# Kernel tuning notes

Measured on AMD Instinct MI355X. Metric: run time of the kernel, lower is better.

## Reference

```python
import jax, jax.numpy as jnp
import numpy as np

EMBED = 1024
HEADS = 16
HEAD_DIM = EMBED // HEADS
LN_EPS = 1e-5
XNORM_GAMMA = 0.01


def xnorm(x, gamma):
    # x * gamma / ||x||_4 along last dim (keepdim)
    norm4 = jnp.sum(x ** 4, axis=-1, keepdims=True) ** 0.25
    return x * gamma / norm4


def setup_inputs() -> dict:
    key = jax.random.key(0)
    ks = jax.random.split(key, 12)
    B, S = 2, 2048
    sc_hd = 1.0 / np.sqrt(HEAD_DIM)
    sc_e = 1.0 / np.sqrt(EMBED)
    return {
        "value": jax.random.normal(ks[0], (B, S, EMBED), jnp.float32),
        "key": jax.random.normal(ks[1], (B, S, EMBED), jnp.float32),
        "query": jax.random.normal(ks[2], (B, S, EMBED), jnp.float32),
        # per-head projections, torch Linear convention: y = x @ W.T
        "Wq": jax.random.normal(ks[3], (HEAD_DIM, HEAD_DIM), jnp.float32) * sc_hd,
        "Wk": jax.random.normal(ks[4], (HEAD_DIM, HEAD_DIM), jnp.float32) * sc_hd,
        "Wv": jax.random.normal(ks[5], (HEAD_DIM, HEAD_DIM), jnp.float32) * sc_hd,
        "Wo": jax.random.normal(ks[6], (EMBED, EMBED), jnp.float32) * sc_e,
        "bo": jnp.zeros((EMBED,), jnp.float32),
        "ln_w": jnp.ones((EMBED,), jnp.float32),
        "ln_b": jnp.zeros((EMBED,), jnp.float32),
        "Wsq": jax.random.normal(ks[7], (EMBED, EMBED), jnp.float32) * sc_e,
        "bsq": jnp.zeros((EMBED,), jnp.float32),
    }


def reference(value, key, query, Wq, Wk, Wv, Wo, bo, ln_w, ln_b, Wsq, bsq):
    B, S, E = query.shape
    # split heads: [B, S, H, D]
    v = value.reshape(B, S, HEADS, HEAD_DIM)
    k = key.reshape(B, S, HEADS, HEAD_DIM)
    q = query.reshape(B, S, HEADS, HEAD_DIM)
    v = jnp.einsum('nshd,ed->nshe', v, Wv)
    k = jnp.einsum('nshd,ed->nshe', k, Wk)
    q = jnp.einsum('nshd,ed->nshe', q, Wq)
    # energy: [B, H, Sq, Sk]
    energy = jnp.einsum('nqhd,nkhd->nhqk', q, k)
    energy_n = xnorm(energy, XNORM_GAMMA)
    v_n = xnorm(v, XNORM_GAMMA)
    out = jnp.einsum('nhql,nlhd->nqhd', energy_n, v_n).reshape(B, S, E)
    attn = out @ Wo.T + bo
    # LayerNorm(attention + query) over embed dim
    x = attn + query
    mu = jnp.mean(x, axis=-1, keepdims=True)
    var = jnp.mean((x - mu) ** 2, axis=-1, keepdims=True)
    x = (x - mu) / jnp.sqrt(var + LN_EPS) * ln_w + ln_b
    # SE gating: x * sigmoid(Linear(x))
    gate = jax.nn.sigmoid(x @ Wsq.T + bsq)
    return x * gate
```

## Files before the change

kernel.cpp:

```cpp
#include <hip/hip_runtime.h>
#include <stdint.h>

#define B_ 2
#define S_ 2048
#define E_ 1024
#define H_ 16
#define HD_ 64
#define N_ (B_*S_)
#define BH_ (B_*H_)
#define GAMMA 0.01f

typedef __attribute__((ext_vector_type(8))) short bf16x8;
typedef __attribute__((ext_vector_type(4))) float f32x4;
typedef __attribute__((ext_vector_type(2))) float f32x2;
typedef __attribute__((ext_vector_type(16))) float f32x16;
typedef __attribute__((ext_vector_type(4))) unsigned int u32x4;
typedef unsigned short u16;
typedef unsigned int u32;

#define SWZ(row, kb) ((kb) ^ (((row)&7)<<4))

__device__ __forceinline__ u16 f2bf(float f){
  union { float f; u32 u; } v; v.f = f;
  return (u16)((v.u + 0x7FFFu + ((v.u>>16)&1u)) >> 16);
}

__device__ __forceinline__ float bf2f(u16 u){
  union { u32 u; float f; } v; v.u = ((u32)u)<<16; return v.f;
}

__device__ __forceinline__ u32 cvt_pk_bf16(float lo, float hi){
  u32 r; asm("v_cvt_pk_bf16_f32 %0, %1, %2" : "=v"(r) : "v"(lo), "v"(hi)); return r;
}

__device__ __forceinline__ uint4 pack8(float4 a, float4 b){
  uint4 r;
  r.x = (u32)f2bf(a.x) | ((u32)f2bf(a.y)<<16);
  r.y = (u32)f2bf(a.z) | ((u32)f2bf(a.w)<<16);
  r.z = (u32)f2bf(b.x) | ((u32)f2bf(b.y)<<16);
  r.w = (u32)f2bf(b.z) | ((u32)f2bf(b.w)<<16);
  return r;
}

__device__ __forceinline__ bf16x8 ldfrag(const unsigned char* base, int row, int kbyte){
  return *reinterpret_cast<const bf16x8*>(base + row*128 + SWZ(row, kbyte));
}
__device__ __forceinline__ bf16x8 ldfragV(const unsigned char* base, int row, int col){
  return *reinterpret_cast<const bf16x8*>(base + row*256 + (col ^ ((row&15)<<4)));
}

__device__ __forceinline__ void gl_lds16(const void* g, void* l){
  __builtin_amdgcn_global_load_lds(
      (const __attribute__((address_space(1))) unsigned int*)g,
      (__attribute__((address_space(3))) unsigned int*)l, 16, 0, 0);
}

__device__ __forceinline__ void proj_mfma(const unsigned char* X, const unsigned char* W,
                                          int wid, int l15, int g4, f32x4 acc[4])
{
  f32x4 z = {0.f,0.f,0.f,0.f};
  acc[0]=z; acc[1]=z; acc[2]=z; acc[3]=z;
  #pragma unroll
  for (int kk=0;kk<2;++kk){
    int kbyte = kk*64 + g4*16;
    bf16x8 a = ldfrag(X, wid*16 + l15, kbyte);
    #pragma unroll
    for (int t=0;t<4;++t){
      bf16x8 w = ldfrag(W, t*16 + l15, kbyte);
      acc[t] = __builtin_amdgcn_mfma_f32_16x16x32_bf16(a, w, acc[t], 0, 0, 0);
    }
  }
}

__global__ __launch_bounds__(256) void k_proj(
    const float* __restrict__ qin, const float* __restrict__ kin, const float* __restrict__ vin,
    const float* __restrict__ Wq, const float* __restrict__ Wk, const float* __restrict__ Wv,
    u16* __restrict__ qp, u16* __restrict__ kp, u16* __restrict__ vnT,
    const float* __restrict__ Wo, const float* __restrict__ Wsq,
    u16* __restrict__ wo16, u16* __restrict__ wsq16)
{
  __shared__ alignas(16) unsigned char sm[57344];
  if (blockIdx.y >= H_){
    int cblk = (blockIdx.y - H_)*64 + blockIdx.x;
    int n4 = (E_*E_)/4;
    for (int i = cblk*256 + threadIdx.x; i < 2*n4; i += 128*256){
      const float4* src; ushort4* dst; int j;
      if (i < n4){ src=(const float4*)Wo;  dst=(ushort4*)wo16;  j=i; }
      else       { src=(const float4*)Wsq; dst=(ushort4*)wsq16; j=i-n4; }
      float4 v = src[j];
      ushort4 p; p.x=f2bf(v.x); p.y=f2bf(v.y); p.z=f2bf(v.z); p.w=f2bf(v.w);
      dst[j] = p;
    }
    return;
  }
  const int XQ=0, XK=8192, XV=16384, WQS=24576, WKS=32768, WVS=40960, VT=49152;
  int tid = threadIdx.x, lane = tid&63, wid = tid>>6;
  int l15 = lane&15, g4 = lane>>4;
  int tb = blockIdx.x*64;
  int h  = blockIdx.y;
  int b  = tb >> 11;
  int sbase = tb & 2047;
  int bh = b*H_ + h;

  {
    int rl = tid>>2;
    int d0 = (tid&3)*16;
    const float* xs[3] = { qin, kin, vin };
    const float* wsrc[3] = { Wq, Wk, Wv };
    const int xoff[3] = {XQ,XK,XV}, woff[3] = {WQS,WKS,WVS};
    #pragma unroll
    for (int m3=0;m3<3;++m3){
      const float4* gx = reinterpret_cast<const float4*>(xs[m3] + (size_t)(tb+rl)*E_ + h*HD_ + d0);
      float4 a=gx[0], bb=gx[1], c=gx[2], d=gx[3];
      *(uint4*)(sm + xoff[m3] + rl*128 + SWZ(rl, d0*2))    = pack8(a,bb);
      *(uint4*)(sm + xoff[m3] + rl*128 + SWZ(rl, d0*2+16)) = pack8(c,d);
      const float4* gw = reinterpret_cast<const float4*>(wsrc[m3] + rl*64 + d0);
      float4 e=gw[0], f=gw[1], g2=gw[2], h2=gw[3];
      *(uint4*)(sm + woff[m3] + rl*128 + SWZ(rl, d0*2))    = pack8(e,f);
      *(uint4*)(sm + woff[m3] + rl*128 + SWZ(rl, d0*2+16)) = pack8(g2,h2);
    }
  }
  __syncthreads();

  f32x4 acc[4];
  proj_mfma(sm+XQ, sm+WQS, wid, l15, g4, acc);
  #pragma unroll
  for (int t=0;t<4;++t)
    #pragma unroll
    for (int r=0;r<4;++r){
      int tokl = wid*16 + g4*4 + r;
      qp[((size_t)bh*S_ + sbase + tokl)*HD_ + t*16 + l15] = f2bf(acc[t][r]);
    }
  proj_mfma(sm+XK, sm+WKS, wid, l15, g4, acc);
  #pragma unroll
  for (int t=0;t<4;++t)
    #pragma unroll
    for (int r=0;r<4;++r){
      int tokl = wid*16 + g4*4 + r;
      kp[((size_t)bh*S_ + sbase + tokl)*HD_ + t*16 + l15] = f2bf(acc[t][r]);
    }
  proj_mfma(sm+XV, sm+WVS, wid, l15, g4, acc);
  {
    float p4r[4] = {0.f,0.f,0.f,0.f};
    #pragma unroll
    for (int t=0;t<4;++t)
      #pragma unroll
      for (int r=0;r<4;++r){ float e = acc[t][r]; float e2 = e*e; p4r[r] += e2*e2; }
    #pragma unroll
    for (int r=0;r<4;++r){
      float p = p4r[r];
      p += __shfl_xor(p,1); p += __shfl_xor(p,2); p += __shfl_xor(p,4); p += __shfl_xor(p,8);
      p4r[r] = GAMMA / sqrtf(sqrtf(p));
    }
    #pragma unroll
    for (int t=0;t<4;++t)
      #pragma unroll
      for (int r=0;r<4;++r){
        int tokl = wid*16 + g4*4 + r;
        int dd = t*16 + l15;
        *(u16*)(sm + VT + dd*128 + SWZ(dd, tokl*2)) = f2bf(acc[t][r] * p4r[r]);
      }
  }
  __syncthreads();
  {
    int dd = tid>>2; int c2 = tid&3;
    size_t gbase = ((size_t)bh*HD_ + dd)*S_ + sbase + c2*16;
    uint4 v0 = *(const uint4*)(sm + VT + dd*128 + SWZ(dd, c2*32));
    uint4 v1 = *(const uint4*)(sm + VT + dd*128 + SWZ(dd, c2*32+16));
    *(uint4*)(vnT + gbase)     = v0;
    *(uint4*)(vnT + gbase + 8) = v1;
  }
}

__global__ __launch_bounds__(256, 2) void k_attn(
    const u16* __restrict__ qp, const u16* __restrict__ kp,
    const u16* __restrict__ vnT, u16* __restrict__ ao)
{
  __shared__ alignas(128) unsigned char sm[65536];
  char* smc = (char*)sm;
  int tid = threadIdx.x, lane = tid&63, wv = tid>>6;
  int l31 = lane&31, hi = lane>>5;
  int qi = wv>>1, kj = wv&1;
  int L = blockIdx.x;
  int xcd = L&7, iw = L>>3;
  int bh = xcd*4 + (iw>>4);
  int qx = iw&15;
  int qb = qx*128;
  int b = bh>>4, h = bh&15;
  const u16* Kb = kp  + (size_t)bh*S_*HD_;
  const u16* Vb = vnT + (size_t)bh*HD_*S_;
  const u16* Qb = qp  + (size_t)bh*S_*HD_;
  int q0 = qb + qi*64;

  bf16x8 qf[2][4];
  #pragma unroll
  for (int f=0;f<2;++f)
    #pragma unroll
    for (int kk=0;kk<4;++kk)
      qf[f][kk] = *reinterpret_cast<const bf16x8*>(Qb + (size_t)(q0 + f*32 + l31)*HD_ + kk*16 + hi*8);

  f32x16 z16 = {};
  f32x16 o[2][2];
  #pragma unroll
  for (int f=0;f<2;++f){ o[f][0] = z16; o[f][1] = z16; }
  f32x2 p4a[2] = {{0.f,0.f},{0.f,0.f}};
  f32x2 p4b[2] = {{0.f,0.f},{0.f,0.f}};

  const char* kSrcC[4]; const char* vSrcC[4];
  #pragma unroll
  for (int c=0;c<4;++c){
    int rk = wv*32 + c*8 + (lane>>3);
    int ck = ((lane&7)*16) ^ ((rk&7)<<4);
    kSrcC[c] = (const char*)Kb + (size_t)rk*128 + ck;
    int rv = wv*16 + c*4 + (lane>>4);
    int cv = ((lane&15)*16) ^ ((rv&15)<<4);
    vSrcC[c] = (const char*)Vb + (size_t)rv*4096 + cv;
  }

  auto STAGE = [&](int bsel, int kt){
    char* db = smc + bsel*32768 + wv*4096;
    #pragma unroll
    for (int c=0;c<4;++c) gl_lds16(kSrcC[c] + (size_t)kt*16384, db + c*1024);
    #pragma unroll
    for (int c=0;c<4;++c) gl_lds16(vSrcC[c] + (size_t)kt*256,   db + 16384 + c*1024);
  };

  auto PACK = [&](const f32x16& e, u32 (&w)[4][2], f32x2& pa){
    #pragma unroll
    for (int j=0;j<8;++j){
      const int g=j>>1, i=j&1;
      float a = e[4*g+2*i], c = e[4*g+2*i+1];
      f32x2 pr = {a, c};
      f32x2 e2;
      asm("v_pk_mul_f32 %0, %1, %1" : "=v"(e2) : "v"(pr));
      asm("v_pk_fma_f32 %0, %1, %1, %0" : "+v"(pa) : "v"(e2));
      w[g][i] = cvt_pk_bf16(a, c);
    }
  };
  auto AFRAG = [&](u32 (&w)[4][2], int s) -> bf16x8 {
    u32 a0 = w[2*s][0], b0 = w[2*s+1][0];
    u32 a1 = w[2*s][1], b1 = w[2*s+1][1];
    asm("v_permlane32_swap_b32 %0, %1" : "+v"(a0), "+v"(b0));
    asm("v_permlane32_swap_b32 %0, %1" : "+v"(a1), "+v"(b1));
    u32x4 fw = {a0, a1, b0, b1};
    return __builtin_bit_cast(bf16x8, fw);
  };

  auto QK = [&](const unsigned char* K_, int s2, f32x16& E0, f32x16& E1){
    bf16x8 ka[4];
    #pragma unroll
    for (int kk=0;kk<4;++kk) ka[kk] = ldfrag(K_, kj*64 + s2*32 + l31, kk*32 + hi*16);
    E0 = z16; E1 = z16;
    __builtin_amdgcn_s_setprio(1);
    #pragma unroll
    for (int kk=0;kk<4;++kk){
      E0 = __builtin_amdgcn_mfma_f32_32x32x16_bf16(ka[kk], qf[0][kk], E0, 0,0,0);
      E1 = __builtin_amdgcn_mfma_f32_32x32x16_bf16(ka[kk], qf[1][kk], E1, 0,0,0);
    }
    __builtin_amdgcn_s_setprio(0);
  };

  auto PVF = [&](const unsigned char* V_, int s2, u32 (&w0)[4][2], u32 (&w1)[4][2]){
    bf16x8 vb[2][2];
    #pragma unroll
    for (int s=0;s<2;++s){
      vb[s][0] = ldfragV(V_, l31,    kj*128 + s2*64 + s*32 + hi*16);
      vb[s][1] = ldfragV(V_, 32+l31, kj*128 + s2*64 + s*32 + hi*16);
    }
    __builtin_amdgcn_s_setprio(1);
    #pragma unroll
    for (int s=0;s<2;++s){
      bf16x8 ef0 = AFRAG(w0, s);
      bf16x8 ef1 = AFRAG(w1, s);
      o[0][0] = __builtin_amdgcn_mfma_f32_32x32x16_bf16(ef0, vb[s][0], o[0][0], 0,0,0);
      o[0][1] = __builtin_amdgcn_mfma_f32_32x32x16_bf16(ef0, vb[s][1], o[0][1], 0,0,0);
      o[1][0] = __builtin_amdgcn_mfma_f32_32x32x16_bf16(ef1, vb[s][0], o[1][0], 0,0,0);
      o[1][1] = __builtin_amdgcn_mfma_f32_32x32x16_bf16(ef1, vb[s][1], o[1][1], 0,0,0);
    }
    __builtin_amdgcn_s_setprio(0);
  };

  const int NT = S_/128;
  STAGE(0, 0); STAGE(1, 1);

  f32x16 eA0, eA1, eB0, eB1;
  u32 wA0[4][2], wA1[4][2], wB0[4][2], wB1[4][2];

  #pragma unroll 1
  for (int t=0; t<NT; ++t){
    if (t < NT-1) { asm volatile("s_waitcnt vmcnt(8)" ::: "memory"); }
    else          { asm volatile("s_waitcnt vmcnt(0)" ::: "memory"); }
    __builtin_amdgcn_s_barrier();
    asm volatile("" ::: "memory");
    const unsigned char* K_ = sm + (t&1)*32768;
    const unsigned char* V_ = K_ + 16384;

    QK(K_, 0, eA0, eA1);
    QK(K_, 1, eB0, eB1);
    PACK(eA0, wA0, p4a[0]);
    PACK(eA1, wA1, p4a[1]);
    PVF(V_, 0, wA0, wA1);
    PACK(eB0, wB0, p4b[0]);
    PACK(eB1, wB1, p4b[1]);
    PVF(V_, 1, wB0, wB1);

    asm volatile("" ::: "memory");
    __builtin_amdgcn_s_barrier();
    asm volatile("" ::: "memory");
    if (t+2 < NT) STAGE(t&1, t+2);
  }

  float p4f[2];
  #pragma unroll
  for (int f=0;f<2;++f) p4f[f] = p4a[f].x + p4a[f].y + p4b[f].x + p4b[f].y;

  __syncthreads();
  float* red  = (float*)smc;
  float* redp = (float*)(smc + 32768);
  if (kj==1){
    #pragma unroll
    for (int f=0;f<2;++f){
      #pragma unroll
      for (int ds=0;ds<2;++ds){
        float* dst = red + ((((qi*2+f)*2+ds)*64 + lane)*16);
        #pragma unroll
        for (int r4=0;r4<4;++r4)
          *(float4*)(dst + r4*4) = make_float4(o[f][ds][r4*4],o[f][ds][r4*4+1],o[f][ds][r4*4+2],o[f][ds][r4*4+3]);
      }
      redp[(qi*2+f)*64 + lane] = p4f[f];
    }
  }
  __syncthreads();
  if (kj==0){
    #pragma unroll
    for (int f=0;f<2;++f){
      #pragma unroll
      for (int ds=0;ds<2;++ds){
        const float* srcp = red + ((((qi*2+f)*2+ds)*64 + lane)*16);
        #pragma unroll
        for (int r4=0;r4<4;++r4){
          float4 t = *(const float4*)(srcp + r4*4);
          o[f][ds][r4*4]+=t.x; o[f][ds][r4*4+1]+=t.y; o[f][ds][r4*4+2]+=t.z; o[f][ds][r4*4+3]+=t.w;
        }
      }
      p4f[f] += redp[(qi*2+f)*64 + lane];
      p4f[f] += __shfl_xor(p4f[f], 32);
    }
    float sc0 = GAMMA * rsqrtf(sqrtf(p4f[0]));
    float sc1 = GAMMA * rsqrtf(sqrtf(p4f[1]));
    #pragma unroll
    for (int f=0;f<2;++f){
      #pragma unroll
      for (int r=0;r<16;++r){
        int qrow = (r&3) + 8*(r>>2) + 4*hi;
        float scr = __shfl(f==0 ? sc0 : sc1, qrow);
        size_t n = (size_t)b*S_ + q0 + f*32 + qrow;
        u16* dst = ao + n*E_ + h*HD_;
        dst[l31]    = f2bf(o[f][0][r] * scr);
        dst[32+l31] = f2bf(o[f][1][r] * scr);
      }
    }
  }
}

template<int MODE>
__global__ __launch_bounds__(256, 2) void k_gemm(
    const u16* __restrict__ A, const u16* __restrict__ Bw,
    const float* __restrict__ bias, const float* __restrict__ auxf,
    const u16* __restrict__ aux16, float* __restrict__ out32, u16* __restrict__ out16)
{
  __shared__ alignas(128) unsigned char sm[73728];
  char* smc = (char*)sm;
  int tid = threadIdx.x, lane = tid&63, wv = tid>>6;
  int l31 = lane&31, hi = lane>>5;
  int wr = wv>>1, wc = wv&1;
  int LL = (blockIdx.x & 7)*64 + (blockIdx.x >> 3);
  int mt = LL >> 4, nt = LL & 15;
  int m0 = mt*128, n0 = nt*64;

  int ric  = lane>>3;
  int colb = ((lane&7)*16) ^ ((ric&7)<<4);
  const char* aSrc[4]; const char* bSrc[2];
  #pragma unroll
  for (int j=0;j<4;++j)
    aSrc[j] = (const char*)A  + ((size_t)(m0 + wv*32 + 8*j + ric)*E_)*2 + colb;
  #pragma unroll
  for (int j=0;j<2;++j)
    bSrc[j] = (const char*)Bw + ((size_t)(n0 + wv*16 + 8*j + ric)*E_)*2 + colb;

  auto STAGE = [&](int bsel, int t){
    char* db = smc + bsel*24576;
    size_t kb2 = (size_t)t*128;
    #pragma unroll
    for (int j=0;j<4;++j) gl_lds16(aSrc[j] + kb2, db + (wv*4+j)*1024);
    #pragma unroll
    for (int j=0;j<2;++j) gl_lds16(bSrc[j] + kb2, db + 16384 + (wv*2+j)*1024);
  };

  f32x16 acc[2] = {{}, {}};

  const int NK = E_/64;
  STAGE(0, 0); STAGE(1, 1);

  #pragma unroll 1
  for (int t=0; t<NK; ++t){
    if (t < NK-1) { asm volatile("s_waitcnt vmcnt(6)" ::: "memory"); }
    else          { asm volatile("s_waitcnt vmcnt(0)" ::: "memory"); }
    __builtin_amdgcn_s_barrier();
    asm volatile("" ::: "memory");
    if (t+2 < NK) STAGE((t+2)%3, t+2);

    const unsigned char* Ap_ = sm + (t%3)*24576;
    const unsigned char* Bp_ = Ap_ + 16384;
    #pragma unroll
    for (int kk=0;kk<4;++kk){
      bf16x8 bfr = ldfrag(Bp_, wc*32 + l31, kk*32 + hi*16);
      bf16x8 af0 = ldfrag(Ap_, wr*64 + l31,      kk*32 + hi*16);
      bf16x8 af1 = ldfrag(Ap_, wr*64 + 32 + l31, kk*32 + hi*16);
      __builtin_amdgcn_s_setprio(1);
      acc[0] = __builtin_amdgcn_mfma_f32_32x32x16_bf16(af0, bfr, acc[0], 0,0,0);
      acc[1] = __builtin_amdgcn_mfma_f32_32x32x16_bf16(af1, bfr, acc[1], 0,0,0);
      __builtin_amdgcn_s_setprio(0);
    }
  }

  int col = n0 + wc*32 + l31;
  float bi = bias[col];
  #pragma unroll
  for (int rg=0;rg<2;++rg)
    #pragma unroll
    for (int r=0;r<16;++r){
      int mrow = m0 + wr*64 + rg*32 + (r&3) + 8*(r>>2) + 4*hi;
      size_t idx = (size_t)mrow*E_ + col;
      float v = acc[rg][r] + bi;
      if (MODE == 0){
        out16[idx] = f2bf(v + auxf[idx]);
      } else {
        float gg = 1.f/(1.f + __expf(-v));
        out32[idx] = bf2f(aux16[idx]) * gg;
      }
    }
}

__global__ __launch_bounds__(256) void k_ln(
    const u16* __restrict__ xin, const float* __restrict__ lnw, const float* __restrict__ lnb,
    u16* __restrict__ xout)
{
  __shared__ float red[8];
  __shared__ float stats[2];
  int row = blockIdx.x, tid = threadIdx.x;
  ushort4 xr = reinterpret_cast<const ushort4*>(xin + (size_t)row*E_)[tid];
  float x0 = bf2f(xr.x), x1 = bf2f(xr.y), x2 = bf2f(xr.z), x3 = bf2f(xr.w);
  float s  = x0 + x1 + x2 + x3;
  float s2 = x0*x0 + x1*x1 + x2*x2 + x3*x3;
  #pragma unroll
  for (int m=1;m<64;m<<=1){ s += __shfl_xor(s,m); s2 += __shfl_xor(s2,m); }
  if ((tid&63)==0){ red[tid>>6] = s; red[4+(tid>>6)] = s2; }
  __syncthreads();
  if (tid==0){
    float ts  = red[0]+red[1]+red[2]+red[3];
    float ts2 = red[4]+red[5]+red[6]+red[7];
    float mu  = ts * (1.f/E_);
    float var = ts2 * (1.f/E_) - mu*mu;
    stats[0] = mu; stats[1] = rsqrtf(var + 1e-5f);
  }
  __syncthreads();
  float mu = stats[0], rstd = stats[1];
  float4 w  = reinterpret_cast<const float4*>(lnw)[tid];
  float4 bb = reinterpret_cast<const float4*>(lnb)[tid];
  ushort4 p;
  p.x = f2bf((x0-mu)*rstd*w.x + bb.x);
  p.y = f2bf((x1-mu)*rstd*w.y + bb.y);
  p.z = f2bf((x2-mu)*rstd*w.z + bb.z);
  p.w = f2bf((x3-mu)*rstd*w.w + bb.w);
  reinterpret_cast<ushort4*>(xout + (size_t)row*E_)[tid] = p;
}

extern "C" void kernel_launch(void* const* d_in, const int* in_sizes, int n_in,
                              void* d_out, int out_size, void* d_ws, size_t ws_size,
                              hipStream_t stream)
{
  const float* value = (const float*)d_in[0];
  const float* key   = (const float*)d_in[1];
  const float* query = (const float*)d_in[2];
  const float* Wq    = (const float*)d_in[3];
  const float* Wk    = (const float*)d_in[4];
  const float* Wv    = (const float*)d_in[5];
  const float* Wo    = (const float*)d_in[6];
  const float* bo    = (const float*)d_in[7];
  const float* lnw   = (const float*)d_in[8];
  const float* lnb   = (const float*)d_in[9];
  const float* Wsq   = (const float*)d_in[10];
  const float* bsq   = (const float*)d_in[11];
  float* out = (float*)d_out;

  char* ws = (char*)d_ws;
  const size_t MB = 1ull<<20;
  u16*   qp     = (u16*)(ws + 0*MB);
  u16*   kp     = (u16*)(ws + 8*MB);
  u16*   vnT    = (u16*)(ws + 16*MB);
  u16*   ao     = (u16*)(ws + 24*MB);
  u16*   xres16 = (u16*)(ws + 8*MB);
  u16*   x16    = (u16*)(ws + 16*MB);
  u16*   wo16   = (u16*)(ws + 48*MB);
  u16*   wsq16  = (u16*)(ws + 50*MB);

  k_proj<<<dim3(N_/64, H_+2), 256, 0, stream>>>(query, key, value, Wq, Wk, Wv,
                                                qp, kp, vnT, Wo, Wsq, wo16, wsq16);
  k_attn<<<512, 256, 0, stream>>>(qp, kp, vnT, ao);
  k_gemm<0><<<512, 256, 0, stream>>>(ao, wo16, bo, query, (const u16*)nullptr, (float*)nullptr, xres16);
  k_ln  <<<N_, 256, 0, stream>>>(xres16, lnw, lnb, x16);
  k_gemm<1><<<512, 256, 0, stream>>>(x16, wsq16, bsq, (const float*)nullptr, x16, out, (u16*)nullptr);
}
```

Measured before the change: 108.6 us.

## Split attention key tiles across four waves per query pair with tree reduction

Doubles the attention block to 512 threads (8 waves), so each of the four key-split waves per query half handles 32 keys per tile instead of 64. Staging of K/V into LDS is spread over more waves, and the split-K partial outputs and norm sums are combined with a two-level LDS reduction. The aim is more waves per CU to hide MFMA and LDS latency, at the cost of extra reduction passes, more barriers, and possible register pressure under launch_bounds(512,4).

```diff
diff --git a/kernel.cpp b/kernel.cpp
--- a/kernel.cpp
+++ b/kernel.cpp
@@ -172,15 +172,16 @@
   }
 }
 
-__global__ __launch_bounds__(256, 2) void k_attn(
+__global__ __launch_bounds__(512, 4) void k_attn(
     const u16* __restrict__ qp, const u16* __restrict__ kp,
     const u16* __restrict__ vnT, u16* __restrict__ ao)
 {
   __shared__ alignas(128) unsigned char sm[65536];
+  __shared__ float p4s[2][256];
   char* smc = (char*)sm;
   int tid = threadIdx.x, lane = tid&63, wv = tid>>6;
   int l31 = lane&31, hi = lane>>5;
-  int qi = wv>>1, kj = wv&1;
+  int qi = wv>>2, kj = wv&3;
   int L = blockIdx.x;
   int xcd = L&7, iw = L>>3;
   int bh = xcd*4 + (iw>>4);
@@ -204,25 +205,23 @@
   #pragma unroll
   for (int f=0;f<2;++f){ o[f][0] = z16; o[f][1] = z16; }
   f32x2 p4a[2] = {{0.f,0.f},{0.f,0.f}};
-  f32x2 p4b[2] = {{0.f,0.f},{0.f,0.f}};
-
-  const char* kSrcC[4]; const char* vSrcC[4];
-  #pragma unroll
-  for (int c=0;c<4;++c){
-    int rk = wv*32 + c*8 + (lane>>3);
-    int ck = ((lane&7)*16) ^ ((rk&7)<<4);
-    kSrcC[c] = (const char*)Kb + (size_t)rk*128 + ck;
-    int rv = wv*16 + c*4 + (lane>>4);
-    int cv = ((lane&15)*16) ^ ((rv&15)<<4);
-    vSrcC[c] = (const char*)Vb + (size_t)rv*4096 + cv;
+
+  const char* kSrcC[2]; const char* vSrcC[2];
+  #pragma unroll
+  for (int c=0;c<2;++c){
+    int off = wv*2048 + c*1024 + lane*16;
+    int rk = off>>7, ck = off&127;
+    kSrcC[c] = (const char*)Kb + (size_t)rk*128 + (ck ^ ((rk&7)<<4));
+    int rv = off>>8, cv = off&255;
+    vSrcC[c] = (const char*)Vb + (size_t)rv*4096 + (cv ^ ((rv&15)<<4));
   }
 
   auto STAGE = [&](int bsel, int kt){
-    char* db = smc + bsel*32768 + wv*4096;
-    #pragma unroll
-    for (int c=0;c<4;++c) gl_lds16(kSrcC[c] + (size_t)kt*16384, db + c*1024);
-    #pragma unroll
-    for (int c=0;c<4;++c) gl_lds16(vSrcC[c] + (size_t)kt*256,   db + 16384 + c*1024);
+    char* db = smc + bsel*32768 + wv*2048;
+    #pragma unroll
+    for (int c=0;c<2;++c) gl_lds16(kSrcC[c] + (size_t)kt*16384, db + c*1024);
+    #pragma unroll
+    for (int c=0;c<2;++c) gl_lds16(vSrcC[c] + (size_t)kt*256,   db + 16384 + c*1024);
   };
 
   auto PACK = [&](const f32x16& e, u32 (&w)[4][2], f32x2& pa){
@@ -246,26 +245,40 @@
     return __builtin_bit_cast(bf16x8, fw);
   };
 
-  auto QK = [&](const unsigned char* K_, int s2, f32x16& E0, f32x16& E1){
+  const int NT = S_/128;
+  STAGE(0, 0); STAGE(1, 1);
+
+  u32 w0[4][2], w1[4][2];
+
+  #pragma unroll 1
+  for (int t=0; t<NT; ++t){
+    if (t < NT-1) { asm volatile("s_waitcnt vmcnt(4)" ::: "memory"); }
+    else          { asm volatile("s_waitcnt vmcnt(0)" ::: "memory"); }
+    __builtin_amdgcn_s_barrier();
+    asm volatile("" ::: "memory");
+    const unsigned char* K_ = sm + (t&1)*32768;
+    const unsigned char* V_ = K_ + 16384;
+
     bf16x8 ka[4];
     #pragma unroll
-    for (int kk=0;kk<4;++kk) ka[kk] = ldfrag(K_, kj*64 + s2*32 + l31, kk*32 + hi*16);
-    E0 = z16; E1 = z16;
+    for (int kk=0;kk<4;++kk) ka[kk] = ldfrag(K_, kj*32 + l31, kk*32 + hi*16);
+    f32x16 e0 = z16, e1 = z16;
     __builtin_amdgcn_s_setprio(1);
     #pragma unroll
     for (int kk=0;kk<4;++kk){
-      E0 = __builtin_amdgcn_mfma_f32_32x32x16_bf16(ka[kk], qf[0][kk], E0, 0,0,0);
-      E1 = __builtin_amdgcn_mfma_f32_32x32x16_bf16(ka[kk], qf[1][kk], E1, 0,0,0);
+      e0 = __builtin_amdgcn_mfma_f32_32x32x16_bf16(ka[kk], qf[0][kk], e0, 0,0,0);
+      e1 = __builtin_amdgcn_mfma_f32_32x32x16_bf16(ka[kk], qf[1][kk], e1, 0,0,0);
     }
     __builtin_amdgcn_s_setprio(0);
-  };
-
-  auto PVF = [&](const unsigned char* V_, int s2, u32 (&w0)[4][2], u32 (&w1)[4][2]){
+
+    PACK(e0, w0, p4a[0]);
+    PACK(e1, w1, p4a[1]);
+
     bf16x8 vb[2][2];
     #pragma unroll
     for (int s=0;s<2;++s){
-      vb[s][0] = ldfragV(V_, l31,    kj*128 + s2*64 + s*32 + hi*16);
-      vb[s][1] = ldfragV(V_, 32+l31, kj*128 + s2*64 + s*32 + hi*16);
+      vb[s][0] = ldfragV(V_, l31,    kj*64 + s*32 + hi*16);
+      vb[s][1] = ldfragV(V_, 32+l31, kj*64 + s*32 + hi*16);
     }
     __builtin_amdgcn_s_setprio(1);
     #pragma unroll
@@ -278,31 +291,6 @@
       o[1][1] = __builtin_amdgcn_mfma_f32_32x32x16_bf16(ef1, vb[s][1], o[1][1], 0,0,0);
     }
     __builtin_amdgcn_s_setprio(0);
-  };
-
-  const int NT = S_/128;
-  STAGE(0, 0); STAGE(1, 1);
-
-  f32x16 eA0, eA1, eB0, eB1;
-  u32 wA0[4][2], wA1[4][2], wB0[4][2], wB1[4][2];
-
-  #pragma unroll 1
-  for (int t=0; t<NT; ++t){
-    if (t < NT-1) { asm volatile("s_waitcnt vmcnt(8)" ::: "memory"); }
-    else          { asm volatile("s_waitcnt vmcnt(0)" ::: "memory"); }
-    __builtin_amdgcn_s_barrier();
-    asm volatile("" ::: "memory");
-    const unsigned char* K_ = sm + (t&1)*32768;
-    const unsigned char* V_ = K_ + 16384;
-
-    QK(K_, 0, eA0, eA1);
-    QK(K_, 1, eB0, eB1);
-    PACK(eA0, wA0, p4a[0]);
-    PACK(eA1, wA1, p4a[1]);
-    PVF(V_, 0, wA0, wA1);
-    PACK(eB0, wB0, p4b[0]);
-    PACK(eB1, wB1, p4b[1]);
-    PVF(V_, 1, wB0, wB1);
 
     asm volatile("" ::: "memory");
     __builtin_amdgcn_s_barrier();
@@ -312,40 +300,52 @@
 
   float p4f[2];
   #pragma unroll
-  for (int f=0;f<2;++f) p4f[f] = p4a[f].x + p4a[f].y + p4b[f].x + p4b[f].y;
-
-  __syncthreads();
-  float* red  = (float*)smc;
-  float* redp = (float*)(smc + 32768);
-  if (kj==1){
+  for (int f=0;f<2;++f) p4f[f] = p4a[f].x + p4a[f].y;
+
+  auto writeO = [&](int sl){
+    float* base = (float*)(smc + sl*32768);
     #pragma unroll
     for (int f=0;f<2;++f){
       #pragma unroll
       for (int ds=0;ds<2;++ds){
-        float* dst = red + ((((qi*2+f)*2+ds)*64 + lane)*16);
+        float* dst = base + ((((qi*2+f)*2+ds)*64 + lane)*16);
         #pragma unroll
         for (int r4=0;r4<4;++r4)
           *(float4*)(dst + r4*4) = make_float4(o[f][ds][r4*4],o[f][ds][r4*4+1],o[f][ds][r4*4+2],o[f][ds][r4*4+3]);
       }
-      redp[(qi*2+f)*64 + lane] = p4f[f];
-    }
-  }
-  __syncthreads();
-  if (kj==0){
+      p4s[sl][(qi*2+f)*64 + lane] = p4f[f];
+    }
+  };
+  auto accO = [&](int sl){
+    const float* base = (const float*)(smc + sl*32768);
     #pragma unroll
     for (int f=0;f<2;++f){
       #pragma unroll
       for (int ds=0;ds<2;++ds){
-        const float* srcp = red + ((((qi*2+f)*2+ds)*64 + lane)*16);
+        const float* srcp = base + ((((qi*2+f)*2+ds)*64 + lane)*16);
         #pragma unroll
         for (int r4=0;r4<4;++r4){
           float4 t = *(const float4*)(srcp + r4*4);
           o[f][ds][r4*4]+=t.x; o[f][ds][r4*4+1]+=t.y; o[f][ds][r4*4+2]+=t.z; o[f][ds][r4*4+3]+=t.w;
         }
       }
-      p4f[f] += redp[(qi*2+f)*64 + lane];
-      p4f[f] += __shfl_xor(p4f[f], 32);
-    }
+      p4f[f] += p4s[sl][(qi*2+f)*64 + lane];
+    }
+  };
+
+  __syncthreads();
+  if (kj==1) writeO(0);
+  if (kj==3) writeO(1);
+  __syncthreads();
+  if (kj==0) accO(0);
+  if (kj==2) accO(1);
+  __syncthreads();
+  if (kj==2) writeO(0);
+  __syncthreads();
+  if (kj==0){
+    accO(0);
+    #pragma unroll
+    for (int f=0;f<2;++f) p4f[f] += __shfl_xor(p4f[f], 32);
     float sc0 = GAMMA * rsqrtf(sqrtf(p4f[0]));
     float sc1 = GAMMA * rsqrtf(sqrtf(p4f[1]));
     #pragma unroll
@@ -507,7 +507,7 @@
 
   k_proj<<<dim3(N_/64, H_+2), 256, 0, stream>>>(query, key, value, Wq, Wk, Wv,
                                                 qp, kp, vnT, Wo, Wsq, wo16, wsq16);
-  k_attn<<<512, 256, 0, stream>>>(qp, kp, vnT, ao);
+  k_attn<<<512, 512, 0, stream>>>(qp, kp, vnT, ao);
   k_gemm<0><<<512, 256, 0, stream>>>(ao, wo16, bo, query, (const u16*)nullptr, (float*)nullptr, xres16);
   k_ln  <<<N_, 256, 0, stream>>>(xres16, lnw, lnb, x16);
   k_gemm<1><<<512, 256, 0, stream>>>(x16, wsq16, bsq, (const float*)nullptr, x16, out, (u16*)nullptr);
```

New measurement: 174.5 us. 1.61x slower.

## Enlarge GEMM tiles to 128x128 with double-buffered LDS staging

Applied to the files above, without the earlier changes.

Both output-projection and gate GEMMs now use 128x128 output tiles instead of 128x64, with each wave computing a 2x2 grid of 32x32 MFMA blocks. This doubles arithmetic per LDS fragment load and halves grid size to 256 blocks. Staging changes from a triple buffer to a double buffer, with an extra barrier before prefetching into the buffer just consumed. The risks are fewer blocks than CUs on the device, which may leave some idle, and less load/compute overlap from the extra barrier.

```diff
diff --git a/kernel.cpp b/kernel.cpp
--- a/kernel.cpp
+++ b/kernel.cpp
@@ -369,77 +369,88 @@
     const float* __restrict__ bias, const float* __restrict__ auxf,
     const u16* __restrict__ aux16, float* __restrict__ out32, u16* __restrict__ out16)
 {
-  __shared__ alignas(128) unsigned char sm[73728];
+  __shared__ alignas(128) unsigned char sm[65536];
   char* smc = (char*)sm;
   int tid = threadIdx.x, lane = tid&63, wv = tid>>6;
   int l31 = lane&31, hi = lane>>5;
   int wr = wv>>1, wc = wv&1;
-  int LL = (blockIdx.x & 7)*64 + (blockIdx.x >> 3);
-  int mt = LL >> 4, nt = LL & 15;
-  int m0 = mt*128, n0 = nt*64;
-
-  int ric  = lane>>3;
-  int colb = ((lane&7)*16) ^ ((ric&7)<<4);
-  const char* aSrc[4]; const char* bSrc[2];
-  #pragma unroll
-  for (int j=0;j<4;++j)
-    aSrc[j] = (const char*)A  + ((size_t)(m0 + wv*32 + 8*j + ric)*E_)*2 + colb;
-  #pragma unroll
-  for (int j=0;j<2;++j)
-    bSrc[j] = (const char*)Bw + ((size_t)(n0 + wv*16 + 8*j + ric)*E_)*2 + colb;
+  int LL = (blockIdx.x & 7)*32 + (blockIdx.x >> 3);
+  int mt = LL >> 3, nt = LL & 7;
+  int m0 = mt*128, n0 = nt*128;
+
+  const char* aS[4]; const char* bS[4];
+  #pragma unroll
+  for (int c=0;c<4;++c){
+    int off = wv*4096 + c*1024 + lane*16;
+    int r = off>>7, cl = off&127;
+    int cs = cl ^ ((r&7)<<4);
+    aS[c] = (const char*)A  + ((size_t)(m0+r)*E_)*2 + cs;
+    bS[c] = (const char*)Bw + ((size_t)(n0+r)*E_)*2 + cs;
+  }
 
   auto STAGE = [&](int bsel, int t){
-    char* db = smc + bsel*24576;
+    char* db = smc + bsel*32768 + wv*4096;
     size_t kb2 = (size_t)t*128;
     #pragma unroll
-    for (int j=0;j<4;++j) gl_lds16(aSrc[j] + kb2, db + (wv*4+j)*1024);
-    #pragma unroll
-    for (int j=0;j<2;++j) gl_lds16(bSrc[j] + kb2, db + 16384 + (wv*2+j)*1024);
+    for (int c=0;c<4;++c) gl_lds16(aS[c] + kb2, db + c*1024);
+    #pragma unroll
+    for (int c=0;c<4;++c) gl_lds16(bS[c] + kb2, db + 16384 + c*1024);
   };
 
-  f32x16 acc[2] = {{}, {}};
+  f32x16 acc[2][2] = {{{}, {}}, {{}, {}}};
 
   const int NK = E_/64;
   STAGE(0, 0); STAGE(1, 1);
 
   #pragma unroll 1
   for (int t=0; t<NK; ++t){
-    if (t < NK-1) { asm volatile("s_waitcnt vmcnt(6)" ::: "memory"); }
+    if (t < NK-1) { asm volatile("s_waitcnt vmcnt(8)" ::: "memory"); }
     else          { asm volatile("s_waitcnt vmcnt(0)" ::: "memory"); }
     __builtin_amdgcn_s_barrier();
     asm volatile("" ::: "memory");
-    if (t+2 < NK) STAGE((t+2)%3, t+2);
-
-    const unsigned char* Ap_ = sm + (t%3)*24576;
+
+    const unsigned char* Ap_ = sm + (t&1)*32768;
     const unsigned char* Bp_ = Ap_ + 16384;
     #pragma unroll
     for (int kk=0;kk<4;++kk){
-      bf16x8 bfr = ldfrag(Bp_, wc*32 + l31, kk*32 + hi*16);
-      bf16x8 af0 = ldfrag(Ap_, wr*64 + l31,      kk*32 + hi*16);
-      bf16x8 af1 = ldfrag(Ap_, wr*64 + 32 + l31, kk*32 + hi*16);
+      int kbyte = kk*32 + hi*16;
+      bf16x8 a0 = ldfrag(Ap_, wr*64 + l31,      kbyte);
+      bf16x8 a1 = ldfrag(Ap_, wr*64 + 32 + l31, kbyte);
+      bf16x8 b0 = ldfrag(Bp_, wc*64 + l31,      kbyte);
+      bf16x8 b1 = ldfrag(Bp_, wc*64 + 32 + l31, kbyte);
       __builtin_amdgcn_s_setprio(1);
-      acc[0] = __builtin_amdgcn_mfma_f32_32x32x16_bf16(af0, bfr, acc[0], 0,0,0);
-      acc[1] = __builtin_amdgcn_mfma_f32_32x32x16_bf16(af1, bfr, acc[1], 0,0,0);
+      acc[0][0] = __builtin_amdgcn_mfma_f32_32x32x16_bf16(a0, b0, acc[0][0], 0,0,0);
+      acc[0][1] = __builtin_amdgcn_mfma_f32_32x32x16_bf16(a0, b1, acc[0][1], 0,0,0);
+      acc[1][0] = __builtin_amdgcn_mfma_f32_32x32x16_bf16(a1, b0, acc[1][0], 0,0,0);
+      acc[1][1] = __builtin_amdgcn_mfma_f32_32x32x16_bf16(a1, b1, acc[1][1], 0,0,0);
       __builtin_amdgcn_s_setprio(0);
     }
-  }
-
-  int col = n0 + wc*32 + l31;
-  float bi = bias[col];
-  #pragma unroll
-  for (int rg=0;rg<2;++rg)
-    #pragma unroll
-    for (int r=0;r<16;++r){
-      int mrow = m0 + wr*64 + rg*32 + (r&3) + 8*(r>>2) + 4*hi;
-      size_t idx = (size_t)mrow*E_ + col;
-      float v = acc[rg][r] + bi;
-      if (MODE == 0){
-        out16[idx] = f2bf(v + auxf[idx]);
-      } else {
-        float gg = 1.f/(1.f + __expf(-v));
-        out32[idx] = bf2f(aux16[idx]) * gg;
+
+    asm volatile("" ::: "memory");
+    __builtin_amdgcn_s_barrier();
+    asm volatile("" ::: "memory");
+    if (t+2 < NK) STAGE(t&1, t+2);
+  }
+
+  #pragma unroll
+  for (int cg=0;cg<2;++cg){
+    int col = n0 + wc*64 + cg*32 + l31;
+    float bi = bias[col];
+    #pragma unroll
+    for (int rg=0;rg<2;++rg)
+      #pragma unroll
+      for (int r=0;r<16;++r){
+        int mrow = m0 + wr*64 + rg*32 + (r&3) + 8*(r>>2) + 4*hi;
+        size_t idx = (size_t)mrow*E_ + col;
+        float v = acc[rg][cg][r] + bi;
+        if (MODE == 0){
+          out16[idx] = f2bf(v + auxf[idx]);
+        } else {
+          float gg = 1.f/(1.f + __expf(-v));
+          out32[idx] = bf2f(aux16[idx]) * gg;
+        }
       }
-    }
+  }
 }
 
 __global__ __launch_bounds__(256) void k_ln(
@@ -508,7 +519,7 @@
   k_proj<<<dim3(N_/64, H_+2), 256, 0, stream>>>(query, key, value, Wq, Wk, Wv,
                                                 qp, kp, vnT, Wo, Wsq, wo16, wsq16);
   k_attn<<<512, 256, 0, stream>>>(qp, kp, vnT, ao);
-  k_gemm<0><<<512, 256, 0, stream>>>(ao, wo16, bo, query, (const u16*)nullptr, (float*)nullptr, xres16);
+  k_gemm<0><<<256, 256, 0, stream>>>(ao, wo16, bo, query, (const u16*)nullptr, (float*)nullptr, xres16);
   k_ln  <<<N_, 256, 0, stream>>>(xres16, lnw, lnb, x16);
-  k_gemm<1><<<512, 256, 0, stream>>>(x16, wsq16, bsq, (const float*)nullptr, x16, out, (u16*)nullptr);
-}
+  k_gemm<1><<<256, 256, 0, stream>>>(x16, wsq16, bsq, (const float*)nullptr, x16, out, (u16*)nullptr);
+}
```

Result: no change. 108.8 us (+0.2%).
